# Optimization experiments

Measured on AMD Instinct MI355X. Metric: run time of the kernel, lower is better.

Reference implementation:

```python
import jax, jax.numpy as jnp
import numpy as np

V = 255      # v_size
L = 16       # l_size = e_size // v_size (row/col weight of cyclic H)
E = V * L    # e_size
P = 8        # num_permu
B = 1024     # batch
CLIP = 10.0


def _build_indices():
    # Synthetic cyclic H: H[i, j] = 1 iff (j - i) % V in S, |S| = L.
    # Reproduces the torch precompute: pos_cyclic_col / pos_cyclic_row edge
    # orderings and the two edge-permutations between them, plus the
    # num_permu codeword permutations (perma).
    rng = np.random.default_rng(0)
    S = np.sort(rng.choice(V, size=L, replace=False))
    U = S                                  # sorted column offsets per row
    T = np.sort((-S) % V)                  # sorted row offsets per column
    m = np.searchsorted(U, (-T) % V)       # row-ordering slot of each col-slot
    C = np.arange(V)[:, None]
    K = np.arange(L)[None, :]
    R = (T[None, :] + C) % V               # row of k-th edge in column c
    idx_c = (C * L + K).ravel()            # edge index in cyclic-col ordering
    idx_r = (R * L + m[None, :]).ravel()   # same edge in cyclic-row ordering
    rc = np.empty(E, np.int32); rc[idx_c] = idx_r   # cycrowtocyccol
    cr = np.empty(E, np.int32); cr[idx_r] = idx_c   # cyccoltocycrow
    perma = np.stack([rng.permutation(V + 1) for _ in range(P)]).astype(np.int32)
    return rc, cr, perma


def setup_inputs() -> dict:
    key = jax.random.key(0)
    ks = jax.random.split(key, 4)
    rc, cr, perma = _build_indices()
    return {
        "x": jax.random.normal(ks[0], (B, V + 1), jnp.float32),
        "message": jnp.zeros((B, P * E), jnp.float32),
        "oddw_v": jax.random.normal(ks[1], (5, L), jnp.float32),
        "oddw_e": jax.random.normal(ks[2], (5, L, L), jnp.float32),
        "w_e_out": jax.random.normal(ks[3], (L,), jnp.float32),
        "perma": jnp.asarray(perma),
        "rc_idx": jnp.asarray(rc),
        "cr_idx": jnp.asarray(cr),
    }


def reference(x, message, oddw_v, oddw_e, w_e_out, perma, rc_idx, cr_idx):
    Bx = x.shape[0]
    dt = x.dtype
    mask_e = 1.0 - jnp.eye(L, dtype=dt)    # zero diagonal (extrinsic mask)
    idx_v = perma[:, 1:]                   # [P, V]: permute rows, drop row 0

    def odd_layer(ev, wv, we):
        # ev: edge messages [B, P, V, L] in cyclic-col edge ordering
        v0 = x[:, :, None] * wv                                  # [B, V+1, L]
        v_out = v0[:, idx_v, :]                                  # [B, P, V, L]
        e = ev.reshape(Bx, P, E)[:, :, rc_idx].reshape(Bx, P, V, L)
        e_intra = jnp.einsum('bpvl,lm->bpvm', e, we * mask_e)
        return jnp.tanh(0.5 * jnp.clip(v_out + e_intra, -CLIP, CLIP))

    def even_layer(o, flag_clip):
        e = o.reshape(Bx, P, E)[:, :, cr_idx].reshape(Bx, P, V, L)
        e = e + (jnp.abs(e) == 0).astype(dt)            # zeros -> 1
        r = jnp.prod(e, axis=-1, keepdims=True) / e     # leave-one-out product
        if flag_clip:
            r = jnp.clip(r, -CLIP, CLIP)
        return jnp.log((1.0 + r) / (1.0 - r + 1e-9) + 1e-9)

    ev = message.reshape(Bx, P, V, L)
    for t in range(5):                     # 5 BP iterations (fixed depth)
        ev = even_layer(odd_layer(ev, oddw_v[t], oddw_e[t]), t == 0)

    # output layer
    e = ev.reshape(Bx, P, E)[:, :, rc_idx].reshape(Bx, P, V, L)
    eo = jnp.einsum('bpvl,l->bpv', e, w_e_out)          # [B, P, V]
    eo = jnp.pad(eo, ((0, 0), (0, 0), (1, 0)))          # zero at position 0
    idx = jnp.broadcast_to(perma[None].astype(jnp.int32), eo.shape)
    total = jnp.take_along_axis(eo, idx, axis=2).sum(axis=1)  # [B, V+1]
    return x + total
```

## Files before the change

kernel.cpp:

```cpp
#include <hip/hip_runtime.h>

#define V 255
#define L 16
#define E (V*L)
#define P 8
#define CLIPV 10.0f

__device__ __forceinline__ float fast_tanh(float x) {
    float e = __expf(2.0f * x);
    return __fdividef(e - 1.0f, e + 1.0f);
}

__device__ __forceinline__ int tr_idx(int i) {
    return (i & (L - 1)) * V + (i >> 4);
}

template <int MODE>
__global__ __launch_bounds__(256) void bp_kernel(
    const float* __restrict__ x,
    const float* __restrict__ msg,
    const float* __restrict__ oddw_v,
    const float* __restrict__ oddw_e,
    const float* __restrict__ w_e_out,
    const int*   __restrict__ perma,
    const int*   __restrict__ rc_idx,
    const int*   __restrict__ cr_idx,
    float* __restrict__ eo_ws,
    const int* __restrict__ invp,
    float* __restrict__ out)
{
    __shared__ float evT[E];
    __shared__ float ooT[E];
    __shared__ float xg[V + 1];
    __shared__ float wm[L * L];
    __shared__ float wvs[L];
    __shared__ float weo[L];

    const int tid = threadIdx.x;
    const int blk = blockIdx.x;
    const int b = blk >> 3;
    const int p = blk & 7;
    const int v = tid;

    if (v < V) {
        const float4* mrow4 = (const float4*)(msg + (size_t)blk * E + v * L);
#pragma unroll
        for (int q = 0; q < 4; ++q) {
            float4 m4 = mrow4[q];
            evT[(4 * q + 0) * V + v] = m4.x;
            evT[(4 * q + 1) * V + v] = m4.y;
            evT[(4 * q + 2) * V + v] = m4.z;
            evT[(4 * q + 3) * V + v] = m4.w;
        }
    }

    const float* xrow = x + b * (V + 1);
    const int* prow = perma + p * (V + 1);
    if (tid < V) xg[tid] = xrow[prow[tid + 1]];
    if (tid < L) weo[tid] = w_e_out[tid];

    int rci[L], cri[L];
    if (v < V) {
#pragma unroll
        for (int l = 0; l < L; ++l) {
            rci[l] = tr_idx(rc_idx[v * L + l]);
            cri[l] = tr_idx(cr_idx[v * L + l]);
        }
    }

    for (int t = 0; t < 5; ++t) {
        {
            int l = tid >> 4, m = tid & 15;
            float w = oddw_e[t * L * L + tid];
            wm[tid] = (l == m) ? 0.0f : w;
            if (tid < L) wvs[tid] = oddw_v[t * L + tid];
        }
        __syncthreads();

        if (v < V) {
            float eg[L];
#pragma unroll
            for (int l = 0; l < L; ++l) eg[l] = evT[rci[l]];
            float s[L];
            const float xv = xg[v];
#pragma unroll
            for (int m = 0; m < L; ++m) s[m] = xv * wvs[m];
#pragma unroll
            for (int l = 0; l < L; ++l) {
                const float el = eg[l];
#pragma unroll
                for (int m = 0; m < L; ++m) s[m] += el * wm[l * L + m];
            }
#pragma unroll
            for (int m = 0; m < L; ++m) {
                float tt = fminf(fmaxf(s[m], -CLIPV), CLIPV);
                ooT[m * V + v] = fast_tanh(0.5f * tt);
            }
        }
        __syncthreads();

        if (v < V) {
            float e2[L];
#pragma unroll
            for (int l = 0; l < L; ++l) {
                float q = ooT[cri[l]];
                e2[l] = (q == 0.0f) ? 1.0f : q;
            }
            float pre[L + 1];
            pre[0] = 1.0f;
#pragma unroll
            for (int l = 0; l < L; ++l) pre[l + 1] = pre[l] * e2[l];
            float suf = 1.0f;
#pragma unroll
            for (int l = L - 1; l >= 0; --l) {
                float r = pre[l] * suf;
                suf *= e2[l];
                if (t == 0) r = fminf(fmaxf(r, -CLIPV), CLIPV);
                float arg = __fdividef(1.0f + r, 1.0f - r + 1e-9f) + 1e-9f;
                evT[l * V + v] = __logf(arg);
            }
        }
        __syncthreads();
    }

    if (v < V) {
        float s = 0.0f;
#pragma unroll
        for (int l = 0; l < L; ++l) s += evT[rci[l]] * weo[l];
        if (MODE == 0) {
            eo_ws[(size_t)blk * V + v] = s;
        } else {
            int jpos = invp[p * (V + 1) + (v + 1)];
            atomicAdd(&out[b * (V + 1) + jpos], s);
        }
    }
}

__global__ __launch_bounds__(256) void out_kernel(
    const float* __restrict__ x,
    const float* __restrict__ eo_ws,
    const int* __restrict__ perma,
    float* __restrict__ out)
{
    const int b = blockIdx.x;
    const int j = threadIdx.x;
    float acc = x[b * (V + 1) + j];
#pragma unroll
    for (int p = 0; p < P; ++p) {
        int idx = perma[p * (V + 1) + j];
        if (idx > 0) acc += eo_ws[((size_t)(b * P + p)) * V + (idx - 1)];
    }
    out[b * (V + 1) + j] = acc;
}

__global__ __launch_bounds__(256) void inv_kernel(const int* __restrict__ perma,
                                                  int* __restrict__ invp)
{
    int p = blockIdx.x, j = threadIdx.x;
    invp[p * (V + 1) + perma[p * (V + 1) + j]] = j;
}

__global__ __launch_bounds__(256) void copy_kernel(const float* __restrict__ x,
                                                   float* __restrict__ out, int n)
{
    int i = blockIdx.x * 256 + threadIdx.x;
    if (i < n) out[i] = x[i];
}

extern "C" void kernel_launch(void* const* d_in, const int* in_sizes, int n_in,
                              void* d_out, int out_size, void* d_ws, size_t ws_size,
                              hipStream_t stream)
{
    const float* x       = (const float*)d_in[0];
    const float* msg     = (const float*)d_in[1];
    const float* oddw_v  = (const float*)d_in[2];
    const float* oddw_e  = (const float*)d_in[3];
    const float* w_e_out = (const float*)d_in[4];
    const int*   perma   = (const int*)d_in[5];
    const int*   rc      = (const int*)d_in[6];
    const int*   cr      = (const int*)d_in[7];
    float* out = (float*)d_out;

    const int Bx = in_sizes[0] / (V + 1);
    const size_t need = (size_t)Bx * P * V * sizeof(float);

    if (ws_size >= need) {
        float* eo = (float*)d_ws;
        hipLaunchKernelGGL((bp_kernel<0>), dim3(Bx * P), dim3(256), 0, stream,
                           x, msg, oddw_v, oddw_e, w_e_out, perma, rc, cr,
                           eo, (const int*)nullptr, (float*)nullptr);
        hipLaunchKernelGGL(out_kernel, dim3(Bx), dim3(256), 0, stream,
                           x, eo, perma, out);
    } else {
        int* invp = (int*)d_ws;
        hipLaunchKernelGGL(inv_kernel, dim3(P), dim3(V + 1), 0, stream, perma, invp);
        hipLaunchKernelGGL(copy_kernel, dim3((out_size + 255) / 256), dim3(256), 0, stream,
                           x, out, out_size);
        hipLaunchKernelGGL((bp_kernel<1>), dim3(Bx * P), dim3(256), 0, stream,
                           x, msg, oddw_v, oddw_e, w_e_out, perma, rc, cr,
                           (float*)nullptr, invp, out);
    }
}
```

Measured before the change: 273.0 us.

## Merge edge buffers into one shared array and preload all layer weights

Replaces the two per-block shared edge buffers with a single buffer, roughly halving LDS use per block so more blocks can be resident per CU. To make the in-place reuse safe, gathers now go into registers, followed by an extra barrier before the buffer is overwritten. All five layers' weights are loaded into shared memory once up front, which removes the per-iteration weight loads and their barrier, and the permuted x value is kept in a register instead of shared memory. The cost is two extra barriers per iteration and somewhat higher register pressure from holding the gathered values across a barrier.

Result: no change. 270.5 us (-0.9%).

```diff
diff --git a/kernel.cpp b/kernel.cpp
--- a/kernel.cpp
+++ b/kernel.cpp
@@ -6,8 +6,8 @@
 #define P 8
 #define CLIPV 10.0f
 
-__device__ __forceinline__ float fast_tanh(float x) {
-    float e = __expf(2.0f * x);
+__device__ __forceinline__ float fast_tanh_half(float t) {
+    float e = __expf(t);
     return __fdividef(e - 1.0f, e + 1.0f);
 }
 
@@ -29,11 +29,9 @@
     const int* __restrict__ invp,
     float* __restrict__ out)
 {
-    __shared__ float evT[E];
-    __shared__ float ooT[E];
-    __shared__ float xg[V + 1];
-    __shared__ float wm[L * L];
-    __shared__ float wvs[L];
+    __shared__ float S[E];
+    __shared__ float wm5[5 * L * L];
+    __shared__ float wvs5[5 * L];
     __shared__ float weo[L];
 
     const int tid = threadIdx.x;
@@ -47,17 +45,26 @@
 #pragma unroll
         for (int q = 0; q < 4; ++q) {
             float4 m4 = mrow4[q];
-            evT[(4 * q + 0) * V + v] = m4.x;
-            evT[(4 * q + 1) * V + v] = m4.y;
-            evT[(4 * q + 2) * V + v] = m4.z;
-            evT[(4 * q + 3) * V + v] = m4.w;
-        }
-    }
-
-    const float* xrow = x + b * (V + 1);
-    const int* prow = perma + p * (V + 1);
-    if (tid < V) xg[tid] = xrow[prow[tid + 1]];
-    if (tid < L) weo[tid] = w_e_out[tid];
+            S[(4 * q + 0) * V + v] = m4.x;
+            S[(4 * q + 1) * V + v] = m4.y;
+            S[(4 * q + 2) * V + v] = m4.z;
+            S[(4 * q + 3) * V + v] = m4.w;
+        }
+    }
+
+    {
+        const int l = tid >> 4, m = tid & 15;
+#pragma unroll
+        for (int t = 0; t < 5; ++t) {
+            float w = oddw_e[t * L * L + tid];
+            wm5[t * L * L + tid] = (l == m) ? 0.0f : w;
+        }
+        if (tid < 5 * L) wvs5[tid] = oddw_v[tid];
+        if (tid < L) weo[tid] = w_e_out[tid];
+    }
+
+    float xv = 0.0f;
+    if (v < V) xv = x[b * (V + 1) + perma[p * (V + 1) + v + 1]];
 
     int rci[L], cri[L];
     if (v < V) {
@@ -68,23 +75,23 @@
         }
     }
 
+    __syncthreads();
+
     for (int t = 0; t < 5; ++t) {
-        {
-            int l = tid >> 4, m = tid & 15;
-            float w = oddw_e[t * L * L + tid];
-            wm[tid] = (l == m) ? 0.0f : w;
-            if (tid < L) wvs[tid] = oddw_v[t * L + tid];
-        }
-        __syncthreads();
-
-        if (v < V) {
-            float eg[L];
-#pragma unroll
-            for (int l = 0; l < L; ++l) eg[l] = evT[rci[l]];
+        const float* wm = &wm5[t * L * L];
+
+        float eg[L];
+        if (v < V) {
+#pragma unroll
+            for (int l = 0; l < L; ++l) eg[l] = S[rci[l]];
+        }
+        __syncthreads();
+
+        if (v < V) {
             float s[L];
-            const float xv = xg[v];
-#pragma unroll
-            for (int m = 0; m < L; ++m) s[m] = xv * wvs[m];
+            const float wv0 = xv;
+#pragma unroll
+            for (int m = 0; m < L; ++m) s[m] = wv0 * wvs5[t * L + m];
 #pragma unroll
             for (int l = 0; l < L; ++l) {
                 const float el = eg[l];
@@ -94,18 +101,22 @@
 #pragma unroll
             for (int m = 0; m < L; ++m) {
                 float tt = fminf(fmaxf(s[m], -CLIPV), CLIPV);
-                ooT[m * V + v] = fast_tanh(0.5f * tt);
-            }
-        }
-        __syncthreads();
-
-        if (v < V) {
-            float e2[L];
+                S[m * V + v] = fast_tanh_half(tt);
+            }
+        }
+        __syncthreads();
+
+        float e2[L];
+        if (v < V) {
 #pragma unroll
             for (int l = 0; l < L; ++l) {
-                float q = ooT[cri[l]];
+                float q = S[cri[l]];
                 e2[l] = (q == 0.0f) ? 1.0f : q;
             }
+        }
+        __syncthreads();
+
+        if (v < V) {
             float pre[L + 1];
             pre[0] = 1.0f;
 #pragma unroll
@@ -117,7 +128,7 @@
                 suf *= e2[l];
                 if (t == 0) r = fminf(fmaxf(r, -CLIPV), CLIPV);
                 float arg = __fdividef(1.0f + r, 1.0f - r + 1e-9f) + 1e-9f;
-                evT[l * V + v] = __logf(arg);
+                S[l * V + v] = __logf(arg);
             }
         }
         __syncthreads();
@@ -126,7 +137,7 @@
     if (v < V) {
         float s = 0.0f;
 #pragma unroll
-        for (int l = 0; l < L; ++l) s += evT[rci[l]] * weo[l];
+        for (int l = 0; l < L; ++l) s += S[rci[l]] * weo[l];
         if (MODE == 0) {
             eo_ws[(size_t)blk * V + v] = s;
         } else {
```
